# Performance work log

Hardware: AMD Instinct MI355X
Metric: run time of the kernel (lower is better)

The kernel has to match this reference:

```python
import jax, jax.numpy as jnp
import numpy as np

EPS = 1e-5  # torch BatchNorm1d default eps


def _bn_train(h, gamma, beta):
    # BatchNorm1d in training mode over the edge (batch) axes: biased variance.
    m = jnp.mean(h, axis=(0, 1), keepdims=True)
    v = jnp.mean(jnp.square(h - m), axis=(0, 1), keepdims=True)
    return (h - m) * jax.lax.rsqrt(v + EPS) * gamma + beta


def setup_inputs() -> dict:
    key = jax.random.key(0)
    ks = jax.random.split(key, 12)
    N, F, H = 1024, 128, 128
    s1 = 1.0 / np.sqrt(2 * F)
    s2 = 1.0 / np.sqrt(H)
    return {
        "x": jax.random.normal(ks[0], (N, F), dtype=jnp.float32),
        "W1": jax.random.uniform(ks[1], (H, 2 * F), jnp.float32, -s1, s1),
        "b1": jax.random.uniform(ks[2], (H,), jnp.float32, -s1, s1),
        "W2": jax.random.uniform(ks[3], (H, H), jnp.float32, -s2, s2),
        "b2": jax.random.uniform(ks[4], (H,), jnp.float32, -s2, s2),
        "W3": jax.random.uniform(ks[5], (1, H), jnp.float32, -s2, s2),
        "b3": jax.random.uniform(ks[6], (1,), jnp.float32, -s2, s2),
        "g1": jnp.ones((H,), jnp.float32),
        "be1": jnp.zeros((H,), jnp.float32),
        "g2": jnp.ones((H,), jnp.float32),
        "be2": jnp.zeros((H,), jnp.float32),
    }


def reference(x, W1, b1, W2, b2, W3, b3, g1, be1, g2, be2):
    N, F = x.shape
    # Edge e = i*N + j pairs [x[j], x[i]] (row=j varies fast, col=i slow).
    # First Linear on the concat splits into two low-rank GEMMs + broadcast add,
    # avoiding the [N^2, 2F] materialization (same math as Linear(concat)).
    Wa, Wb = W1[:, :F], W1[:, F:]
    A = x @ Wa.T            # contribution of x[row] = x[j] -> varies over axis 1
    B = x @ Wb.T            # contribution of x[col] = x[i] -> varies over axis 0
    h = A[None, :, :] + B[:, None, :] + b1      # [N, N, H], h[i, j]
    h = jax.nn.relu(_bn_train(h, g1, be1))
    h = jnp.einsum('ijh,kh->ijk', h, W2) + b2   # [N, N, H]
    h = jax.nn.relu(_bn_train(h, g2, be2))
    logits = jnp.einsum('ijh,kh->ijk', h, W3)[..., 0] + b3[0]  # [N, N]
    adj = jax.nn.sigmoid((logits + logits.T) * 0.5)
    adj = adj - jnp.diag(jnp.diag(adj))
    return adj
```

## Files before the change

kernel.cpp:

```cpp
#include <hip/hip_runtime.h>
#include <hip/hip_bf16.h>

typedef _Float16 f16x8 __attribute__((ext_vector_type(8)));
typedef _Float16 f16x4 __attribute__((ext_vector_type(4)));
typedef float    f32x4 __attribute__((ext_vector_type(4)));

#define EPSV 1e-5f

__global__ __launch_bounds__(256) void k_ab(const float* __restrict__ x,
                                            const float* __restrict__ W1,
                                            const float* __restrict__ W2,
                                            float* __restrict__ A,
                                            float* __restrict__ Bm,
                                            float* __restrict__ gs,
                                            unsigned int* __restrict__ w2p) {
  __shared__ float xs[4 * 128];
  int t = threadIdx.x;
  if (blockIdx.x >= 256) {
    int c = (blockIdx.x - 256) * 256 + t;
    int pair = c & 3;
    int col  = (c >> 2) & 15;
    int quad = (c >> 6) & 3;
    int nt   = (c >> 8) & 7;
    int ks   = (c >> 11) & 3;
    int k = nt * 16 + col;
    int hch = ks * 32 + quad * 8 + pair * 2;
    _Float16 b0 = (_Float16)W2[k * 128 + hch];
    _Float16 b1 = (_Float16)W2[k * 128 + hch + 1];
    unsigned int u0 = *(unsigned short*)&b0, u1 = *(unsigned short*)&b1;
    w2p[c] = u0 | (u1 << 16);
    return;
  }
  int j0 = blockIdx.x * 4;
  for (int idx = t; idx < 512; idx += 256) xs[idx] = x[j0 * 128 + idx];
  __syncthreads();
  int h = t & 127, half = t >> 7;
  const float4* wrow = (const float4*)(W1 + h * 256 + half * 128);
  const float4* xs4 = (const float4*)xs;
  float a0 = 0.f, a1 = 0.f, a2 = 0.f, a3 = 0.f;
#pragma unroll 8
  for (int ch = 0; ch < 32; ++ch) {
    float4 wv = wrow[ch];
    float4 x0 = xs4[ch], x1 = xs4[32 + ch], x2 = xs4[64 + ch], x3 = xs4[96 + ch];
    a0 += wv.x * x0.x + wv.y * x0.y + wv.z * x0.z + wv.w * x0.w;
    a1 += wv.x * x1.x + wv.y * x1.y + wv.z * x1.z + wv.w * x1.w;
    a2 += wv.x * x2.x + wv.y * x2.y + wv.z * x2.z + wv.w * x2.w;
    a3 += wv.x * x3.x + wv.y * x3.y + wv.z * x3.z + wv.w * x3.w;
  }
  float* dst = half ? Bm : A;
  dst[(j0 + 0) * 128 + h] = a0;
  dst[(j0 + 1) * 128 + h] = a1;
  dst[(j0 + 2) * 128 + h] = a2;
  dst[(j0 + 3) * 128 + h] = a3;
  float s = a0 + a1 + a2 + a3;
  float q = a0 * a0 + a1 * a1 + a2 * a2 + a3 * a3;
  atomicAdd(&gs[half * 256 + h], s);
  atomicAdd(&gs[half * 256 + 128 + h], q);
}

__global__ __launch_bounds__(256) void k_fold_apply(const float* __restrict__ gs,
                                                    const float* __restrict__ g1,
                                                    const float* __restrict__ be1,
                                                    const float* __restrict__ A,
                                                    const float* __restrict__ Bm,
                                                    unsigned int* __restrict__ Apf,
                                                    unsigned int* __restrict__ Btf) {
  __shared__ float sc_s[128], ta_s[128], tb_s[128];
  int t = threadIdx.x;
  if (t < 128) {
    const float inv = 1.f / 1024.f;
    float mA = gs[t] * inv;
    float vA = gs[128 + t] * inv - mA * mA;
    float mB = gs[256 + t] * inv;
    float vB = gs[384 + t] * inv - mB * mB;
    float sc = g1[t] * rsqrtf(vA + vB + EPSV);
    sc_s[t] = sc;
    ta_s[t] = be1[t] - mA * sc;
    tb_s[t] = -mB * sc;
  }
  __syncthreads();
  int idx4 = blockIdx.x * 256 + t;
  int c4 = idx4 & 31;
  f32x4 sc = ((const f32x4*)sc_s)[c4];
  f32x4 ta = ((const f32x4*)ta_s)[c4];
  f32x4 tb = ((const f32x4*)tb_s)[c4];
  f32x4 a = ((const f32x4*)A)[idx4];
  f32x4 b = ((const f32x4*)Bm)[idx4];
  f32x4 oa = a * sc + ta;
  f32x4 ob = b * sc + tb;
  f16x4 oah = __builtin_convertvector(oa, f16x4);
  f16x4 obh = __builtin_convertvector(ob, f16x4);
  int j = idx4 >> 5;
  int h4 = c4 << 2;
  int S = j >> 6, s = (j >> 4) & 3, col = j & 15;
  int ks = h4 >> 5, quad = (h4 >> 3) & 3, e0 = h4 & 7;
  int au = S * 4096 + ((s * 4 + ks) * 64 + quad * 16 + col) * 4 + (e0 >> 1);
  *(uint2*)(Apf + au) = *(uint2*)&oah;
  *(uint2*)(Btf + idx4 * 2) = *(uint2*)&obh;
}

template <int PASS>
__global__ __launch_bounds__(256) void k_pass(
    const unsigned int* __restrict__ Apf, const unsigned int* __restrict__ Btf,
    const unsigned int* __restrict__ w2p,
    float* __restrict__ sum2, const float* __restrict__ g2,
    const float* __restrict__ be2, const float* __restrict__ W3v,
    const float* __restrict__ b3p, float* __restrict__ L) {
  __shared__ unsigned int ats[4096];
  __shared__ float red[1024];
  int t = threadIdx.x;
  int bid = blockIdx.x;
  int bj = bid & 15, bi = bid >> 4;
  int lane = t & 63, w = t >> 6;
  int col = lane & 15, quad = lane >> 4;

  const unsigned int* atsrc = Apf + bj * 4096;
#pragma unroll
  for (int it = 0; it < 4; ++it) {
    int g = w * 4 + it;
    __builtin_amdgcn_global_load_lds(
        (const __attribute__((address_space(1))) unsigned int*)(atsrc + g * 256 + lane * 4),
        (__attribute__((address_space(3))) unsigned int*)(ats + g * 256),
        16, 0, 0);
  }

  f16x8 btr[2][4];
  {
    int i0 = bi * 8 + w * 2;
#pragma unroll
    for (int r = 0; r < 2; ++r)
#pragma unroll
      for (int ks = 0; ks < 4; ++ks)
        btr[r][ks] = *(const f16x8*)((const _Float16*)Btf + (i0 + r) * 128 + ks * 32 + quad * 8);
  }

  f16x8 bw[4][8];
#pragma unroll
  for (int ks = 0; ks < 4; ++ks)
#pragma unroll
    for (int nt = 0; nt < 8; ++nt)
      bw[ks][nt] = *(const f16x8*)((const _Float16*)w2p + (((ks * 8 + nt) * 64) + lane) * 8);

  float s1[8], s2[8];
  float al[8], uu[8], w3l[8];
  float b3v = 0.f;
  if (PASS == 1) {
#pragma unroll
    for (int nt = 0; nt < 8; ++nt) { s1[nt] = 0.f; s2[nt] = 0.f; }
  } else {
    b3v = b3p[0];
    const float invM = 1.f / (1024.f * 1024.f);
#pragma unroll
    for (int nt = 0; nt < 8; ++nt) {
      int k = nt * 16 + col;
      float mdot = sum2[k] * invM;
      float var = sum2[128 + k] * invM - mdot * mdot;
      float alv = g2[k] * rsqrtf(var + EPSV);
      al[nt] = alv;
      uu[nt] = be2[k] - mdot * alv;
      w3l[nt] = W3v[k];
    }
  }
  __syncthreads();

  const f16x8 zz = {(_Float16)0, (_Float16)0, (_Float16)0, (_Float16)0,
                    (_Float16)0, (_Float16)0, (_Float16)0, (_Float16)0};

  for (int s = 0; s < 4; ++s) {
    f32x4 acc[2][8];
#pragma unroll
    for (int mt = 0; mt < 2; ++mt)
#pragma unroll
      for (int nt = 0; nt < 8; ++nt) acc[mt][nt] = (f32x4){0.f, 0.f, 0.f, 0.f};

#pragma unroll
    for (int ks = 0; ks < 4; ++ks) {
      f16x8 af = *(const f16x8*)(ats + ((s * 4 + ks) * 64 + lane) * 4);
      f16x8 a0 = __builtin_elementwise_max(af + btr[0][ks], zz);
      f16x8 a1 = __builtin_elementwise_max(af + btr[1][ks], zz);
#pragma unroll
      for (int nt = 0; nt < 8; ++nt) {
        acc[0][nt] = __builtin_amdgcn_mfma_f32_16x16x32_f16(a0, bw[ks][nt], acc[0][nt], 0, 0, 0);
        acc[1][nt] = __builtin_amdgcn_mfma_f32_16x16x32_f16(a1, bw[ks][nt], acc[1][nt], 0, 0, 0);
      }
    }

    if (PASS == 1) {
#pragma unroll
      for (int nt = 0; nt < 8; ++nt)
#pragma unroll
        for (int mt = 0; mt < 2; ++mt)
#pragma unroll
          for (int r = 0; r < 4; ++r) {
            float d = acc[mt][nt][r];
            s1[nt] += d;
            s2[nt] = fmaf(d, d, s2[nt]);
          }
    } else {
#pragma unroll
      for (int mt = 0; mt < 2; ++mt) {
        float rsum[4] = {0.f, 0.f, 0.f, 0.f};
#pragma unroll
        for (int nt = 0; nt < 8; ++nt)
#pragma unroll
          for (int r = 0; r < 4; ++r) {
            float h = fmaxf(fmaf(acc[mt][nt][r], al[nt], uu[nt]), 0.f);
            rsum[r] = fmaf(h, w3l[nt], rsum[r]);
          }
#pragma unroll
        for (int r = 0; r < 4; ++r) {
          rsum[r] += __shfl_xor(rsum[r], 1);
          rsum[r] += __shfl_xor(rsum[r], 2);
          rsum[r] += __shfl_xor(rsum[r], 4);
          rsum[r] += __shfl_xor(rsum[r], 8);
        }
        if (col == 0) {
          int i = bi * 8 + w * 2 + mt;
          float4 v = make_float4(rsum[0] + b3v, rsum[1] + b3v,
                                 rsum[2] + b3v, rsum[3] + b3v);
          *(float4*)(&L[i * 1024 + bj * 64 + s * 16 + quad * 4]) = v;
        }
      }
    }
  }

  if (PASS == 1) {
#pragma unroll
    for (int nt = 0; nt < 8; ++nt) {
      s1[nt] += __shfl_xor(s1[nt], 16);
      s1[nt] += __shfl_xor(s1[nt], 32);
      s2[nt] += __shfl_xor(s2[nt], 16);
      s2[nt] += __shfl_xor(s2[nt], 32);
    }
    if (lane < 16) {
#pragma unroll
      for (int nt = 0; nt < 8; ++nt) {
        red[w * 256 + nt * 16 + lane] = s1[nt];
        red[w * 256 + 128 + nt * 16 + lane] = s2[nt];
      }
    }
    __syncthreads();
    float tot = red[t] + red[256 + t] + red[512 + t] + red[768 + t];
    atomicAdd(&sum2[t], tot);
  }
}

__global__ __launch_bounds__(256) void k_adj(const float* __restrict__ L,
                                             float* __restrict__ out) {
  int idx = blockIdx.x * 256 + threadIdx.x;
  int i = idx >> 10, j = idx & 1023;
  float a = L[i * 1024 + j];
  float b = L[j * 1024 + i];
  float s = 1.f / (1.f + __expf(-0.5f * (a + b)));
  out[idx] = (i == j) ? 0.f : s;
}

extern "C" void kernel_launch(void* const* d_in, const int* in_sizes, int n_in,
                              void* d_out, int out_size, void* d_ws, size_t ws_size,
                              hipStream_t stream) {
  const float* x   = (const float*)d_in[0];
  const float* W1  = (const float*)d_in[1];
  const float* W2  = (const float*)d_in[3];
  const float* W3  = (const float*)d_in[5];
  const float* b3  = (const float*)d_in[6];
  const float* g1  = (const float*)d_in[7];
  const float* be1 = (const float*)d_in[8];
  const float* g2  = (const float*)d_in[9];
  const float* be2 = (const float*)d_in[10];

  float* ws = (float*)d_ws;
  float* A          = ws;
  float* Bm         = ws + 131072;
  unsigned int* Apf = (unsigned int*)(ws + 262144);
  unsigned int* Btf = (unsigned int*)(ws + 327680);
  unsigned int* w2p = (unsigned int*)(ws + 393216);
  float* gs         = ws + 401408;
  float* sum2       = ws + 401920;
  float* L          = ws + 402176;
  float* out        = (float*)d_out;

  hipMemsetAsync(gs, 0, 768 * sizeof(float), stream);

  k_ab<<<288, 256, 0, stream>>>(x, W1, W2, A, Bm, gs, w2p);
  k_fold_apply<<<128, 256, 0, stream>>>(gs, g1, be1, A, Bm, Apf, Btf);
  k_pass<1><<<2048, 256, 0, stream>>>(Apf, Btf, w2p, sum2, nullptr, nullptr, nullptr, nullptr, nullptr);
  k_pass<2><<<2048, 256, 0, stream>>>(Apf, Btf, w2p, sum2, g2, be2, W3, b3, L);
  k_adj<<<4096, 256, 0, stream>>>(L, out);
}
```

Baseline: 217.4 us.

## Fuse BN1 fold/apply into pass kernels and double per-block column tile

Removes the separate fold/apply kernel: k_ab now writes raw A/B projections directly in fp16 in the MFMA fragment layout, and each pass kernel computes the BN1 scale/shift from the global sums and applies it in LDS and registers after loading. Each pass block now covers 128 j-columns instead of 64, halving the grid and reusing the loaded B/W2 registers across more MFMA work. This saves one launch and an fp32 round trip through global memory. In exchange, the BN1 affine is recomputed redundantly in every block, raw pre-BN values are rounded to fp16 before normalization (a precision change), and LDS use per block grows.

```diff
diff --git a/kernel.cpp b/kernel.cpp
--- a/kernel.cpp
+++ b/kernel.cpp
@@ -10,8 +10,8 @@
 __global__ __launch_bounds__(256) void k_ab(const float* __restrict__ x,
                                             const float* __restrict__ W1,
                                             const float* __restrict__ W2,
-                                            float* __restrict__ A,
-                                            float* __restrict__ Bm,
+                                            _Float16* __restrict__ Apf,
+                                            _Float16* __restrict__ Btf,
                                             float* __restrict__ gs,
                                             unsigned int* __restrict__ w2p) {
   __shared__ float xs[4 * 128];
@@ -47,26 +47,65 @@
     a2 += wv.x * x2.x + wv.y * x2.y + wv.z * x2.z + wv.w * x2.w;
     a3 += wv.x * x3.x + wv.y * x3.y + wv.z * x3.z + wv.w * x3.w;
   }
-  float* dst = half ? Bm : A;
-  dst[(j0 + 0) * 128 + h] = a0;
-  dst[(j0 + 1) * 128 + h] = a1;
-  dst[(j0 + 2) * 128 + h] = a2;
-  dst[(j0 + 3) * 128 + h] = a3;
+  if (half == 0) {
+    int S = j0 >> 7, s = (j0 >> 4) & 7, colb = j0 & 15;
+    int ks = h >> 5, quad = (h >> 3) & 3, eh = (h >> 2) & 1, pos = h & 3;
+    int base = S * 16384 + ((s * 4 + ks) * 64 + quad * 16 + colb) * 8 + eh * 4 + pos;
+    Apf[base]      = (_Float16)a0;
+    Apf[base + 8]  = (_Float16)a1;
+    Apf[base + 16] = (_Float16)a2;
+    Apf[base + 24] = (_Float16)a3;
+  } else {
+    Btf[(j0 + 0) * 128 + h] = (_Float16)a0;
+    Btf[(j0 + 1) * 128 + h] = (_Float16)a1;
+    Btf[(j0 + 2) * 128 + h] = (_Float16)a2;
+    Btf[(j0 + 3) * 128 + h] = (_Float16)a3;
+  }
   float s = a0 + a1 + a2 + a3;
   float q = a0 * a0 + a1 * a1 + a2 * a2 + a3 * a3;
   atomicAdd(&gs[half * 256 + h], s);
   atomicAdd(&gs[half * 256 + 128 + h], q);
 }
 
-__global__ __launch_bounds__(256) void k_fold_apply(const float* __restrict__ gs,
-                                                    const float* __restrict__ g1,
-                                                    const float* __restrict__ be1,
-                                                    const float* __restrict__ A,
-                                                    const float* __restrict__ Bm,
-                                                    unsigned int* __restrict__ Apf,
-                                                    unsigned int* __restrict__ Btf) {
-  __shared__ float sc_s[128], ta_s[128], tb_s[128];
+__device__ __forceinline__ void f16x8_to_f32(f16x8 v, f32x4& lo, f32x4& hi) {
+  f16x4 l4 = __builtin_shufflevector(v, v, 0, 1, 2, 3);
+  f16x4 h4 = __builtin_shufflevector(v, v, 4, 5, 6, 7);
+  lo = __builtin_convertvector(l4, f32x4);
+  hi = __builtin_convertvector(h4, f32x4);
+}
+__device__ __forceinline__ f16x8 f32_to_f16x8(f32x4 lo, f32x4 hi) {
+  f16x4 l4 = __builtin_convertvector(lo, f16x4);
+  f16x4 h4 = __builtin_convertvector(hi, f16x4);
+  return __builtin_shufflevector(l4, h4, 0, 1, 2, 3, 4, 5, 6, 7);
+}
+
+template <int PASS>
+__global__ __launch_bounds__(256) void k_pass(
+    const _Float16* __restrict__ Apf, const _Float16* __restrict__ Btf,
+    const unsigned int* __restrict__ w2p,
+    const float* __restrict__ gs, const float* __restrict__ g1,
+    const float* __restrict__ be1,
+    float* __restrict__ sum2, const float* __restrict__ g2,
+    const float* __restrict__ be2, const float* __restrict__ W3v,
+    const float* __restrict__ b3p, float* __restrict__ L) {
+  __shared__ unsigned int ats[8192];
+  __shared__ float red[1024];
   int t = threadIdx.x;
+  int bid = blockIdx.x;
+  int bj = bid & 7, bi = bid >> 3;
+  int lane = t & 63, w = t >> 6;
+  int col = lane & 15, quad = lane >> 4;
+
+  const unsigned int* atsrc = (const unsigned int*)Apf + bj * 8192;
+#pragma unroll
+  for (int it = 0; it < 8; ++it) {
+    int g = w * 8 + it;
+    __builtin_amdgcn_global_load_lds(
+        (const __attribute__((address_space(1))) unsigned int*)(atsrc + g * 256 + lane * 4),
+        (__attribute__((address_space(3))) unsigned int*)(ats + g * 256),
+        16, 0, 0);
+  }
+
   if (t < 128) {
     const float inv = 1.f / 1024.f;
     float mA = gs[t] * inv;
@@ -74,64 +113,9 @@
     float mB = gs[256 + t] * inv;
     float vB = gs[384 + t] * inv - mB * mB;
     float sc = g1[t] * rsqrtf(vA + vB + EPSV);
-    sc_s[t] = sc;
-    ta_s[t] = be1[t] - mA * sc;
-    tb_s[t] = -mB * sc;
-  }
-  __syncthreads();
-  int idx4 = blockIdx.x * 256 + t;
-  int c4 = idx4 & 31;
-  f32x4 sc = ((const f32x4*)sc_s)[c4];
-  f32x4 ta = ((const f32x4*)ta_s)[c4];
-  f32x4 tb = ((const f32x4*)tb_s)[c4];
-  f32x4 a = ((const f32x4*)A)[idx4];
-  f32x4 b = ((const f32x4*)Bm)[idx4];
-  f32x4 oa = a * sc + ta;
-  f32x4 ob = b * sc + tb;
-  f16x4 oah = __builtin_convertvector(oa, f16x4);
-  f16x4 obh = __builtin_convertvector(ob, f16x4);
-  int j = idx4 >> 5;
-  int h4 = c4 << 2;
-  int S = j >> 6, s = (j >> 4) & 3, col = j & 15;
-  int ks = h4 >> 5, quad = (h4 >> 3) & 3, e0 = h4 & 7;
-  int au = S * 4096 + ((s * 4 + ks) * 64 + quad * 16 + col) * 4 + (e0 >> 1);
-  *(uint2*)(Apf + au) = *(uint2*)&oah;
-  *(uint2*)(Btf + idx4 * 2) = *(uint2*)&obh;
-}
-
-template <int PASS>
-__global__ __launch_bounds__(256) void k_pass(
-    const unsigned int* __restrict__ Apf, const unsigned int* __restrict__ Btf,
-    const unsigned int* __restrict__ w2p,
-    float* __restrict__ sum2, const float* __restrict__ g2,
-    const float* __restrict__ be2, const float* __restrict__ W3v,
-    const float* __restrict__ b3p, float* __restrict__ L) {
-  __shared__ unsigned int ats[4096];
-  __shared__ float red[1024];
-  int t = threadIdx.x;
-  int bid = blockIdx.x;
-  int bj = bid & 15, bi = bid >> 4;
-  int lane = t & 63, w = t >> 6;
-  int col = lane & 15, quad = lane >> 4;
-
-  const unsigned int* atsrc = Apf + bj * 4096;
-#pragma unroll
-  for (int it = 0; it < 4; ++it) {
-    int g = w * 4 + it;
-    __builtin_amdgcn_global_load_lds(
-        (const __attribute__((address_space(1))) unsigned int*)(atsrc + g * 256 + lane * 4),
-        (__attribute__((address_space(3))) unsigned int*)(ats + g * 256),
-        16, 0, 0);
-  }
-
-  f16x8 btr[2][4];
-  {
-    int i0 = bi * 8 + w * 2;
-#pragma unroll
-    for (int r = 0; r < 2; ++r)
-#pragma unroll
-      for (int ks = 0; ks < 4; ++ks)
-        btr[r][ks] = *(const f16x8*)((const _Float16*)Btf + (i0 + r) * 128 + ks * 32 + quad * 8);
+    red[t] = sc;
+    red[128 + t] = be1[t] - mA * sc;
+    red[256 + t] = -mB * sc;
   }
 
   f16x8 bw[4][8];
@@ -141,13 +125,9 @@
     for (int nt = 0; nt < 8; ++nt)
       bw[ks][nt] = *(const f16x8*)((const _Float16*)w2p + (((ks * 8 + nt) * 64) + lane) * 8);
 
-  float s1[8], s2[8];
   float al[8], uu[8], w3l[8];
   float b3v = 0.f;
-  if (PASS == 1) {
-#pragma unroll
-    for (int nt = 0; nt < 8; ++nt) { s1[nt] = 0.f; s2[nt] = 0.f; }
-  } else {
+  if (PASS == 2) {
     b3v = b3p[0];
     const float invM = 1.f / (1024.f * 1024.f);
 #pragma unroll
@@ -163,10 +143,56 @@
   }
   __syncthreads();
 
+  {
+    int h0 = ((t >> 6) & 3) * 32 + ((t >> 4) & 3) * 8;
+    f32x4 scl = *(const f32x4*)(red + h0);
+    f32x4 sch = *(const f32x4*)(red + h0 + 4);
+    f32x4 tal = *(const f32x4*)(red + 128 + h0);
+    f32x4 tah = *(const f32x4*)(red + 128 + h0 + 4);
+#pragma unroll
+    for (int k = 0; k < 8; ++k) {
+      unsigned int* p = ats + t * 4 + k * 1024;
+      f16x8 v = *(f16x8*)p;
+      f32x4 lo, hi;
+      f16x8_to_f32(v, lo, hi);
+      lo = lo * scl + tal;
+      hi = hi * sch + tah;
+      *(f16x8*)p = f32_to_f16x8(lo, hi);
+    }
+  }
+
+  f16x8 btr[2][4];
+  {
+    int i0 = bi * 8 + w * 2;
+#pragma unroll
+    for (int r = 0; r < 2; ++r)
+#pragma unroll
+      for (int ks = 0; ks < 4; ++ks) {
+        int hh = ks * 32 + quad * 8;
+        f16x8 braw = *(const f16x8*)(Btf + (i0 + r) * 128 + hh);
+        f32x4 lo, hi;
+        f16x8_to_f32(braw, lo, hi);
+        f32x4 sl = *(const f32x4*)(red + hh);
+        f32x4 sh = *(const f32x4*)(red + hh + 4);
+        f32x4 tl = *(const f32x4*)(red + 256 + hh);
+        f32x4 th = *(const f32x4*)(red + 256 + hh + 4);
+        lo = lo * sl + tl;
+        hi = hi * sh + th;
+        btr[r][ks] = f32_to_f16x8(lo, hi);
+      }
+  }
+  __syncthreads();
+
+  float s1[8], s2[8];
+  if (PASS == 1) {
+#pragma unroll
+    for (int nt = 0; nt < 8; ++nt) { s1[nt] = 0.f; s2[nt] = 0.f; }
+  }
+
   const f16x8 zz = {(_Float16)0, (_Float16)0, (_Float16)0, (_Float16)0,
                     (_Float16)0, (_Float16)0, (_Float16)0, (_Float16)0};
 
-  for (int s = 0; s < 4; ++s) {
+  for (int s = 0; s < 8; ++s) {
     f32x4 acc[2][8];
 #pragma unroll
     for (int mt = 0; mt < 2; ++mt)
@@ -218,7 +244,7 @@
           int i = bi * 8 + w * 2 + mt;
           float4 v = make_float4(rsum[0] + b3v, rsum[1] + b3v,
                                  rsum[2] + b3v, rsum[3] + b3v);
-          *(float4*)(&L[i * 1024 + bj * 64 + s * 16 + quad * 4]) = v;
+          *(float4*)(&L[i * 1024 + bj * 128 + s * 16 + quad * 4]) = v;
         }
       }
     }
@@ -232,6 +258,7 @@
       s2[nt] += __shfl_xor(s2[nt], 16);
       s2[nt] += __shfl_xor(s2[nt], 32);
     }
+    __syncthreads();
     if (lane < 16) {
 #pragma unroll
       for (int nt = 0; nt < 8; ++nt) {
@@ -269,21 +296,20 @@
   const float* be2 = (const float*)d_in[10];
 
   float* ws = (float*)d_ws;
-  float* A          = ws;
-  float* Bm         = ws + 131072;
-  unsigned int* Apf = (unsigned int*)(ws + 262144);
-  unsigned int* Btf = (unsigned int*)(ws + 327680);
-  unsigned int* w2p = (unsigned int*)(ws + 393216);
-  float* gs         = ws + 401408;
-  float* sum2       = ws + 401920;
-  float* L          = ws + 402176;
+  _Float16* Apf     = (_Float16*)ws;
+  _Float16* Btf     = (_Float16*)(ws + 65536);
+  unsigned int* w2p = (unsigned int*)(ws + 131072);
+  float* gs         = ws + 139264;
+  float* sum2       = ws + 139776;
+  float* L          = ws + 140032;
   float* out        = (float*)d_out;
 
   hipMemsetAsync(gs, 0, 768 * sizeof(float), stream);
 
-  k_ab<<<288, 256, 0, stream>>>(x, W1, W2, A, Bm, gs, w2p);
-  k_fold_apply<<<128, 256, 0, stream>>>(gs, g1, be1, A, Bm, Apf, Btf);
-  k_pass<1><<<2048, 256, 0, stream>>>(Apf, Btf, w2p, sum2, nullptr, nullptr, nullptr, nullptr, nullptr);
-  k_pass<2><<<2048, 256, 0, stream>>>(Apf, Btf, w2p, sum2, g2, be2, W3, b3, L);
+  k_ab<<<288, 256, 0, stream>>>(x, W1, W2, Apf, Btf, gs, w2p);
+  k_pass<1><<<1024, 256, 0, stream>>>(Apf, Btf, w2p, gs, g1, be1, sum2,
+                                      nullptr, nullptr, nullptr, nullptr, nullptr);
+  k_pass<2><<<1024, 256, 0, stream>>>(Apf, Btf, w2p, gs, g1, be1, sum2,
+                                      g2, be2, W3, b3, L);
   k_adj<<<4096, 256, 0, stream>>>(L, out);
 }
```

New measurement: 207.4 us. 4.6% less time.
